# Kernel optimization log

Hardware: AMD Instinct MI355X
Metric: run time of the kernel (lower is better)

Reference implementation:

```python
import jax, jax.numpy as jnp
import numpy as np

N_NODES = 100000
N_EDGES = 3200000
N_FEAT = 128
HIDDEN = 64
N_CLASSES = 3
N_GRAPHS = 512
BN_EPS = 1e-5


def setup_inputs() -> dict:
    key = jax.random.key(0)
    ks = jax.random.split(key, 16)
    x = jax.random.normal(ks[0], (N_NODES, N_FEAT), dtype=jnp.float32)
    edge_index = jax.random.randint(ks[1], (2, N_EDGES), 0, N_NODES, dtype=jnp.int64)
    batch = jnp.sort(jax.random.randint(ks[2], (N_NODES,), 0, N_GRAPHS, dtype=jnp.int64))
    # GCNConv weights (glorot-ish scale), biases
    W1 = jax.random.normal(ks[3], (N_FEAT, HIDDEN), dtype=jnp.float32) / np.sqrt(N_FEAT)
    b1 = jnp.zeros((HIDDEN,), dtype=jnp.float32)
    W2 = jax.random.normal(ks[4], (HIDDEN, HIDDEN), dtype=jnp.float32) / np.sqrt(HIDDEN)
    b2 = jnp.zeros((HIDDEN,), dtype=jnp.float32)
    # BatchNorm params + running stats (eval mode)
    g1 = jnp.ones((HIDDEN,), dtype=jnp.float32)
    bt1 = jnp.zeros((HIDDEN,), dtype=jnp.float32)
    rm1 = jax.random.normal(ks[5], (HIDDEN,), dtype=jnp.float32) * 0.1
    rv1 = jax.random.uniform(ks[6], (HIDDEN,), dtype=jnp.float32) + 0.5
    g2 = jnp.ones((HIDDEN,), dtype=jnp.float32)
    bt2 = jnp.zeros((HIDDEN,), dtype=jnp.float32)
    rm2 = jax.random.normal(ks[7], (HIDDEN,), dtype=jnp.float32) * 0.1
    rv2 = jax.random.uniform(ks[8], (HIDDEN,), dtype=jnp.float32) + 0.5
    # classifier
    Wc = jax.random.normal(ks[9], (HIDDEN, N_CLASSES), dtype=jnp.float32) / np.sqrt(HIDDEN)
    bc = jnp.zeros((N_CLASSES,), dtype=jnp.float32)
    return dict(x=x, W1=W1, b1=b1, g1=g1, bt1=bt1, rm1=rm1, rv1=rv1,
                W2=W2, b2=b2, g2=g2, bt2=bt2, rm2=rm2, rv2=rv2,
                Wc=Wc, bc=bc, edge_index=edge_index, batch=batch)


def _gcn_conv(x, W, b, src, dst):
    # x' = D^{-1/2} (A + I) D^{-1/2} X W + b  (PyG GCNConv with self-loops)
    n = x.shape[0]
    h = x @ W  # [N, H]
    loops = jnp.arange(n, dtype=src.dtype)
    s = jnp.concatenate([src, loops])
    d = jnp.concatenate([dst, loops])
    deg = jax.ops.segment_sum(jnp.ones_like(d, dtype=h.dtype), d, num_segments=n)
    dinv = jnp.where(deg > 0, jax.lax.rsqrt(deg), 0.0)
    norm = dinv[s] * dinv[d]  # [E+N]
    msg = h[s] * norm[:, None]  # gather + scale
    out = jax.ops.segment_sum(msg, d, num_segments=n)  # scatter-add
    return out + b


def _bn_eval(x, gamma, beta, rmean, rvar):
    return (x - rmean) * jax.lax.rsqrt(rvar + BN_EPS) * gamma + beta


def reference(x, W1, b1, g1, bt1, rm1, rv1, W2, b2, g2, bt2, rm2, rv2, Wc, bc, edge_index, batch):
    src, dst = edge_index[0], edge_index[1]
    h = _gcn_conv(x, W1, b1, src, dst)
    h = jax.nn.relu(_bn_eval(h, g1, bt1, rm1, rv1))
    # dropout inactive in eval mode
    h = _gcn_conv(h, W2, b2, src, dst)
    h = jax.nn.relu(_bn_eval(h, g2, bt2, rm2, rv2))
    # global mean pool over graphs
    sums = jax.ops.segment_sum(h, batch, num_segments=N_GRAPHS)
    cnts = jax.ops.segment_sum(jnp.ones((h.shape[0],), dtype=h.dtype), batch, num_segments=N_GRAPHS)
    pooled = sums / jnp.maximum(cnts, 1.0)[:, None]  # [G, H]
    return pooled @ Wc + bc  # [G, C]
```

## Files before the change

### kernel.cpp

```cpp
#include <hip/hip_runtime.h>

#define NN 100000
#define NE 3200000
#define NG 512
#define NCB 782
#define BN_EPS 1e-5f

typedef unsigned short u16;
typedef unsigned int u32;

__device__ __forceinline__ u16 f2bf(float f) {
    u32 u = __float_as_uint(f);
    u += 0x7FFF + ((u >> 16) & 1);
    return (u16)(u >> 16);
}

__global__ __launch_bounds__(256) void k_chist(const int* __restrict__ dst, int* __restrict__ ccount) {
    __shared__ int h[NCB];
    int t = threadIdx.x;
    for (int i = t; i < NCB; i += 256) h[i] = 0;
    __syncthreads();
    int stride = gridDim.x * 256;
    for (int e = blockIdx.x * 256 + t; e < NE; e += stride)
        atomicAdd(&h[dst[e] >> 7], 1);
    __syncthreads();
    for (int i = t; i < NCB; i += 256)
        if (h[i]) atomicAdd(&ccount[i], h[i]);
}

__global__ __launch_bounds__(256) void k_cscan(const int* __restrict__ ccount, int* __restrict__ cbase,
                                               int* __restrict__ fbase, int* __restrict__ gcur) {
    __shared__ int sh[256], sh2[256];
    int t = threadIdx.x;
    int v[4], w[4];
    int s = 0, s2 = 0;
#pragma unroll
    for (int j = 0; j < 4; j++) {
        int idx = t * 4 + j;
        int c = (idx < NCB) ? ccount[idx] : 0;
        v[j] = c;
        w[j] = (idx < NCB) ? ((c + 387) & ~3) : 0;
        s += v[j]; s2 += w[j];
    }
    sh[t] = s; sh2[t] = s2;
    __syncthreads();
    for (int off = 1; off < 256; off <<= 1) {
        int x = (t >= off) ? sh[t - off] : 0;
        int x2 = (t >= off) ? sh2[t - off] : 0;
        __syncthreads();
        sh[t] += x; sh2[t] += x2;
        __syncthreads();
    }
    int run = sh[t] - s, run2 = sh2[t] - s2;
#pragma unroll
    for (int j = 0; j < 4; j++) {
        int idx = t * 4 + j;
        if (idx < NCB) { cbase[idx] = run; gcur[idx] = run; fbase[idx] = run2; }
        run += v[j]; run2 += w[j];
    }
    if (t == 255) cbase[NCB] = run;
}

#define P1_CHUNK 16384
__global__ __launch_bounds__(1024) void k_p1(const int* __restrict__ src, const int* __restrict__ dst,
                                             int* __restrict__ gcur, int* __restrict__ esc) {
    __shared__ int ccur[NCB];
    const int t = threadIdx.x;
    const int e0 = blockIdx.x * P1_CHUNK;
    for (int i = t; i < NCB; i += 1024) ccur[i] = 0;
    __syncthreads();
    int n = NE - e0; if (n > P1_CHUNK) n = P1_CHUNK;
    for (int idx = t; idx < n; idx += 1024)
        atomicAdd(&ccur[dst[e0 + idx] >> 7], 1);
    __syncthreads();
    for (int i = t; i < NCB; i += 1024) {
        int c = ccur[i];
        ccur[i] = (c > 0) ? atomicAdd(&gcur[i], c) : 0;
    }
    __syncthreads();
    for (int idx = t; idx < n; idx += 1024) {
        int dd = dst[e0 + idx];
        int s = src[e0 + idx];
        int pos = atomicAdd(&ccur[dd >> 7], 1);
        esc[pos] = s | ((dd & 127) << 17);
    }
}

__global__ __launch_bounds__(256) void k_p2(const int* __restrict__ esc, const int* __restrict__ cbase,
                                            const int* __restrict__ fbase, int* __restrict__ esf,
                                            int* __restrict__ offs, int* __restrict__ cntp,
                                            float* __restrict__ dinv) {
    __shared__ int lcnt[128], loff[128], lcur[128];
    int t = threadIdx.x, b = blockIdx.x;
    int c0 = cbase[b], c1 = cbase[b + 1];
    if (t < 128) lcnt[t] = 0;
    __syncthreads();
    for (int i = c0 + t; i < c1; i += 256) atomicAdd(&lcnt[esc[i] >> 17], 1);
    __syncthreads();
    int p = 0, cnt = 0;
    if (t < 128) { cnt = lcnt[t]; p = (cnt + 3) & ~3; loff[t] = p; }
    __syncthreads();
    for (int off = 1; off < 128; off <<= 1) {
        int x = (t >= off && t < 128) ? loff[t - off] : 0;
        __syncthreads();
        if (t < 128) loff[t] += x;
        __syncthreads();
    }
    int fb = fbase[b];
    int node = (b << 7) + t;
    if (t < 128) {
        int o = fb + loff[t] - p;
        lcur[t] = o;
        if (node < NN) {
            offs[node] = o;
            cntp[node] = p;
            dinv[node] = rsqrtf((float)(cnt + 1));
            for (int q = cnt; q < p; q++) esf[o + q] = NN;
        }
    }
    __syncthreads();
    for (int i = c0 + t; i < c1; i += 256) {
        int rec = esc[i];
        int pos = atomicAdd(&lcur[rec >> 17], 1);
        esf[pos] = rec & 0x1FFFF;
    }
}

template <int K>
__global__ __launch_bounds__(256) void k_gemm(const float* __restrict__ X,
                                              const float* __restrict__ W,
                                              const float* __restrict__ dinv,
                                              u16* __restrict__ hp, int M) {
    __shared__ float xs[128 * 68];
    __shared__ float ws[64 * 64];
    const int t = threadIdx.x;
    const int row0 = blockIdx.x * 128;
    const int rg = t >> 3;
    const int f0 = (t & 7) * 8;

    float acc[4][8];
#pragma unroll
    for (int j = 0; j < 4; j++)
#pragma unroll
        for (int c = 0; c < 8; c++) acc[j][c] = 0.0f;

    for (int kc = 0; kc < K; kc += 64) {
        __syncthreads();
        const float4* Wg = (const float4*)(W + (size_t)kc * 64);
        float4* ws4 = (float4*)ws;
#pragma unroll
        for (int i = 0; i < 4; i++) ws4[t + i * 256] = Wg[t + i * 256];
#pragma unroll
        for (int p = 0; p < 8; p++) {
            int rr = p * 16 + (t >> 4);
            int c4 = (t & 15) * 4;
            int row = row0 + rr;
            float4 v = make_float4(0.f, 0.f, 0.f, 0.f);
            if (row < M) v = *(const float4*)(X + (size_t)row * K + kc + c4);
            *(float4*)(&xs[rr * 68 + c4]) = v;
        }
        __syncthreads();

        for (int kk = 0; kk < 64; kk += 4) {
            float4 xv[4];
#pragma unroll
            for (int j = 0; j < 4; j++)
                xv[j] = *(const float4*)(&xs[(rg + 32 * j) * 68 + kk]);
#pragma unroll
            for (int kki = 0; kki < 4; kki++) {
                float4 w0 = *(const float4*)(&ws[(kk + kki) * 64 + f0]);
                float4 w1 = *(const float4*)(&ws[(kk + kki) * 64 + f0 + 4]);
#pragma unroll
                for (int j = 0; j < 4; j++) {
                    float a = (&xv[j].x)[kki];
                    acc[j][0] = fmaf(a, w0.x, acc[j][0]);
                    acc[j][1] = fmaf(a, w0.y, acc[j][1]);
                    acc[j][2] = fmaf(a, w0.z, acc[j][2]);
                    acc[j][3] = fmaf(a, w0.w, acc[j][3]);
                    acc[j][4] = fmaf(a, w1.x, acc[j][4]);
                    acc[j][5] = fmaf(a, w1.y, acc[j][5]);
                    acc[j][6] = fmaf(a, w1.z, acc[j][6]);
                    acc[j][7] = fmaf(a, w1.w, acc[j][7]);
                }
            }
        }
    }

#pragma unroll
    for (int j = 0; j < 4; j++) {
        int row = row0 + rg + 32 * j;
        if (row < M) {
            float di = dinv[row];
            uint4 pk;
            pk.x = (u32)f2bf(acc[j][0] * di) | ((u32)f2bf(acc[j][1] * di) << 16);
            pk.y = (u32)f2bf(acc[j][2] * di) | ((u32)f2bf(acc[j][3] * di) << 16);
            pk.z = (u32)f2bf(acc[j][4] * di) | ((u32)f2bf(acc[j][5] * di) << 16);
            pk.w = (u32)f2bf(acc[j][6] * di) | ((u32)f2bf(acc[j][7] * di) << 16);
            *(uint4*)(hp + (size_t)row * 64 + f0) = pk;
        }
    }
}

__global__ __launch_bounds__(256) void k_agg(const u32* __restrict__ hp2,
                                             const int* __restrict__ esf,
                                             const int* __restrict__ offs,
                                             const int* __restrict__ cntp,
                                             const float* __restrict__ dinv,
                                             const float* __restrict__ bias,
                                             const float* __restrict__ gam,
                                             const float* __restrict__ bet,
                                             const float* __restrict__ rm,
                                             const float* __restrict__ rv,
                                             float* __restrict__ out) {
    const int lane = threadIdx.x & 63;
    const int half = lane >> 5;
    const int fp = lane & 31;
    const int node = (blockIdx.x * 256 + threadIdx.x) >> 6;
    if (node >= NN) return;
    const int beg = offs[node];
    const int mp = cntp[node];
    float ax = 0.0f, ay = 0.0f;
    for (int c = 0; c < mp; c += 64) {
        int m = mp - c;
        if (m > 64) m = 64;
        int rec = (lane < m) ? esf[beg + c + lane] : NN;
        int j = 0;
        for (; j + 16 <= m; j += 16) {
            u32 v[8];
#pragma unroll
            for (int u = 0; u < 8; u++) {
                int s = __shfl(rec, j + 2 * u + half);
                v[u] = hp2[(size_t)s * 32 + fp];
            }
#pragma unroll
            for (int u = 0; u < 8; u++) {
                ax += __uint_as_float(v[u] << 16);
                ay += __uint_as_float(v[u] & 0xFFFF0000u);
            }
        }
        for (; j < m; j += 4) {
            int s0 = __shfl(rec, j + half);
            int s1 = __shfl(rec, j + 2 + half);
            u32 v0 = hp2[(size_t)s0 * 32 + fp];
            u32 v1 = hp2[(size_t)s1 * 32 + fp];
            ax += __uint_as_float(v0 << 16);
            ay += __uint_as_float(v0 & 0xFFFF0000u);
            ax += __uint_as_float(v1 << 16);
            ay += __uint_as_float(v1 & 0xFFFF0000u);
        }
    }
    ax += __shfl_xor(ax, 32);
    ay += __shfl_xor(ay, 32);
    u32 sv = hp2[(size_t)node * 32 + fp];
    ax += __uint_as_float(sv << 16);
    ay += __uint_as_float(sv & 0xFFFF0000u);

    const float di = dinv[node];
    const int f0 = fp * 2;
    float2 bia = *(const float2*)(bias + f0);
    float2 ga  = *(const float2*)(gam + f0);
    float2 be  = *(const float2*)(bet + f0);
    float2 rme = *(const float2*)(rm + f0);
    float2 rva = *(const float2*)(rv + f0);
    float vx = ax * di + bia.x;
    float vy = ay * di + bia.y;
    float yx = (vx - rme.x) * (ga.x * rsqrtf(rva.x + BN_EPS)) + be.x;
    float yy = (vy - rme.y) * (ga.y * rsqrtf(rva.y + BN_EPS)) + be.y;
    if (half == 0)
        *(float2*)(out + (size_t)node * 64 + f0) = make_float2(fmaxf(yx, 0.0f), fmaxf(yy, 0.0f));
}

__global__ __launch_bounds__(256) void k_poolcls(const float* __restrict__ h,
                                                 const int* __restrict__ batch,
                                                 const float* __restrict__ Wc,
                                                 const float* __restrict__ bc,
                                                 float* __restrict__ out) {
    __shared__ float sh[256];
    const int g = blockIdx.x;
    const int t = threadIdx.x;
    const int lane = t & 63;
    const int wv = t >> 6;
    int lo = 0, hi = NN;
    while (lo < hi) { int mid = (lo + hi) >> 1; if (batch[mid] < g) lo = mid + 1; else hi = mid; }
    const int r0 = lo;
    hi = NN;
    while (lo < hi) { int mid = (lo + hi) >> 1; if (batch[mid] < g + 1) lo = mid + 1; else hi = mid; }
    const int r1 = lo;
    float acc = 0.0f;
    for (int r = r0 + wv; r < r1; r += 4)
        acc += h[(size_t)r * 64 + lane];
    sh[t] = acc;
    __syncthreads();
    if (wv == 0) {
        float p = sh[lane] + sh[64 + lane] + sh[128 + lane] + sh[192 + lane];
        p *= 1.0f / fmaxf((float)(r1 - r0), 1.0f);
        float c0 = p * Wc[lane * 3 + 0];
        float c1 = p * Wc[lane * 3 + 1];
        float c2 = p * Wc[lane * 3 + 2];
        for (int o = 32; o > 0; o >>= 1) {
            c0 += __shfl_xor(c0, o);
            c1 += __shfl_xor(c1, o);
            c2 += __shfl_xor(c2, o);
        }
        if (lane == 0) {
            out[g * 3 + 0] = c0 + bc[0];
            out[g * 3 + 1] = c1 + bc[1];
            out[g * 3 + 2] = c2 + bc[2];
        }
    }
}

extern "C" void kernel_launch(void* const* d_in, const int* in_sizes, int n_in,
                              void* d_out, int out_size, void* d_ws, size_t ws_size,
                              hipStream_t stream) {
    const float* x   = (const float*)d_in[0];
    const float* W1  = (const float*)d_in[1];
    const float* b1  = (const float*)d_in[2];
    const float* g1  = (const float*)d_in[3];
    const float* bt1 = (const float*)d_in[4];
    const float* rm1 = (const float*)d_in[5];
    const float* rv1 = (const float*)d_in[6];
    const float* W2  = (const float*)d_in[7];
    const float* b2  = (const float*)d_in[8];
    const float* g2  = (const float*)d_in[9];
    const float* bt2 = (const float*)d_in[10];
    const float* rm2 = (const float*)d_in[11];
    const float* rv2 = (const float*)d_in[12];
    const float* Wc  = (const float*)d_in[13];
    const float* bc  = (const float*)d_in[14];
    const int* ei    = (const int*)d_in[15];
    const int* batch = (const int*)d_in[16];
    const int* srcp = ei;
    const int* dstp = ei + NE;

    char* ws = (char*)d_ws;
    u16*   hpb    = (u16*)(ws);
    int*   ccount = (int*)(ws + 12800128);
    int*   cbase  = (int*)(ws + 12803264);
    int*   fbase  = (int*)(ws + 12806400);
    int*   gcur   = (int*)(ws + 12809536);
    int*   offs   = (int*)(ws + 12812672);
    int*   cntp   = (int*)(ws + 13212672);
    float* dinv   = (float*)(ws + 13612672);
    int*   esf    = (int*)(ws + 14012672);
    float* bufB   = (float*)(ws + 28052672);
    int*   esc    = (int*)(ws + 28052672);

    hipMemsetAsync(hpb + (size_t)NN * 64, 0, 128 + NCB * 4, stream);

    k_chist<<<512, 256, 0, stream>>>(dstp, ccount);
    k_cscan<<<1, 256, 0, stream>>>(ccount, cbase, fbase, gcur);
    k_p1<<<(NE + P1_CHUNK - 1) / P1_CHUNK, 1024, 0, stream>>>(srcp, dstp, gcur, esc);
    k_p2<<<NCB, 256, 0, stream>>>(esc, cbase, fbase, esf, offs, cntp, dinv);

    k_gemm<128><<<(NN + 127) / 128, 256, 0, stream>>>(x, W1, dinv, hpb, NN);
    k_agg<<<(NN * 64 + 255) / 256, 256, 0, stream>>>((const u32*)hpb, esf, offs, cntp, dinv, b1, g1, bt1, rm1, rv1, bufB);

    k_gemm<64><<<(NN + 127) / 128, 256, 0, stream>>>(bufB, W2, dinv, hpb, NN);
    k_agg<<<(NN * 64 + 255) / 256, 256, 0, stream>>>((const u32*)hpb, esf, offs, cntp, dinv, b2, g2, bt2, rm2, rv2, bufB);

    k_poolcls<<<NG, 256, 0, stream>>>(bufB, batch, Wc, bc, (float*)d_out);
}
```

Baseline: 394.4 us.

## Fuse CSR build kernels into one cooperative kernel with grid syncs

Replaces the four graph-build kernels (coarse histogram, scan, coarse scatter, fine bucket sort) with a single cooperative kernel of 196 blocks of 1024 threads. Grid-wide barriers separate the phases. The per-block histogram is kept in shared memory and reused for the scatter pass, so dst is read once fewer. In the fine phase each block handles four coarse buckets with 256-thread subgroups. The aim is to remove launch gaps and a redundant pass. The cost is grid.sync overhead, lower parallelism in phase 2 (196 blocks instead of 782), and a single-block scan.

Measured after the change: 488.9 us. 24.0% more time.

```diff
diff --git a/kernel.cpp b/kernel.cpp
--- a/kernel.cpp
+++ b/kernel.cpp
@@ -1,4 +1,7 @@
 #include <hip/hip_runtime.h>
+#include <hip/hip_cooperative_groups.h>
+
+namespace cg = cooperative_groups;
 
 #define NN 100000
 #define NE 3200000
@@ -6,6 +9,9 @@
 #define NCB 782
 #define BN_EPS 1e-5f
 
+#define BCHUNK 16384
+#define NBLK 196
+
 typedef unsigned short u16;
 typedef unsigned int u32;
 
@@ -15,114 +21,106 @@
     return (u16)(u >> 16);
 }
 
-__global__ __launch_bounds__(256) void k_chist(const int* __restrict__ dst, int* __restrict__ ccount) {
-    __shared__ int h[NCB];
-    int t = threadIdx.x;
-    for (int i = t; i < NCB; i += 256) h[i] = 0;
+__global__ __launch_bounds__(1024) void k_build(const int* __restrict__ src, const int* __restrict__ dst,
+                                                int* __restrict__ ccount, int* __restrict__ cbase,
+                                                int* __restrict__ fbase, int* __restrict__ gcur,
+                                                int* __restrict__ esc, int* __restrict__ esf,
+                                                int* __restrict__ offs, int* __restrict__ cntp,
+                                                float* __restrict__ dinv) {
+    __shared__ int lhist[NCB];
+    __shared__ int buf[2048];
+    cg::grid_group grid = cg::this_grid();
+    const int t = threadIdx.x;
+    const int b = blockIdx.x;
+    const int e0 = b * BCHUNK;
+    int n = NE - e0; if (n > BCHUNK) n = BCHUNK; if (n < 0) n = 0;
+
+    for (int i = t; i < NCB; i += 1024) lhist[i] = 0;
     __syncthreads();
-    int stride = gridDim.x * 256;
-    for (int e = blockIdx.x * 256 + t; e < NE; e += stride)
-        atomicAdd(&h[dst[e] >> 7], 1);
+    for (int idx = t; idx < n; idx += 1024)
+        atomicAdd(&lhist[dst[e0 + idx] >> 7], 1);
     __syncthreads();
-    for (int i = t; i < NCB; i += 256)
-        if (h[i]) atomicAdd(&ccount[i], h[i]);
-}
-
-__global__ __launch_bounds__(256) void k_cscan(const int* __restrict__ ccount, int* __restrict__ cbase,
-                                               int* __restrict__ fbase, int* __restrict__ gcur) {
-    __shared__ int sh[256], sh2[256];
-    int t = threadIdx.x;
-    int v[4], w[4];
-    int s = 0, s2 = 0;
-#pragma unroll
-    for (int j = 0; j < 4; j++) {
-        int idx = t * 4 + j;
-        int c = (idx < NCB) ? ccount[idx] : 0;
-        v[j] = c;
-        w[j] = (idx < NCB) ? ((c + 387) & ~3) : 0;
-        s += v[j]; s2 += w[j];
-    }
-    sh[t] = s; sh2[t] = s2;
-    __syncthreads();
-    for (int off = 1; off < 256; off <<= 1) {
-        int x = (t >= off) ? sh[t - off] : 0;
-        int x2 = (t >= off) ? sh2[t - off] : 0;
-        __syncthreads();
-        sh[t] += x; sh2[t] += x2;
-        __syncthreads();
-    }
-    int run = sh[t] - s, run2 = sh2[t] - s2;
-#pragma unroll
-    for (int j = 0; j < 4; j++) {
-        int idx = t * 4 + j;
-        if (idx < NCB) { cbase[idx] = run; gcur[idx] = run; fbase[idx] = run2; }
-        run += v[j]; run2 += w[j];
-    }
-    if (t == 255) cbase[NCB] = run;
-}
-
-#define P1_CHUNK 16384
-__global__ __launch_bounds__(1024) void k_p1(const int* __restrict__ src, const int* __restrict__ dst,
-                                             int* __restrict__ gcur, int* __restrict__ esc) {
-    __shared__ int ccur[NCB];
-    const int t = threadIdx.x;
-    const int e0 = blockIdx.x * P1_CHUNK;
-    for (int i = t; i < NCB; i += 1024) ccur[i] = 0;
-    __syncthreads();
-    int n = NE - e0; if (n > P1_CHUNK) n = P1_CHUNK;
-    for (int idx = t; idx < n; idx += 1024)
-        atomicAdd(&ccur[dst[e0 + idx] >> 7], 1);
-    __syncthreads();
+    for (int i = t; i < NCB; i += 1024)
+        if (lhist[i]) atomicAdd(&ccount[i], lhist[i]);
+
+    grid.sync();
+
+    if (b == 0) {
+        int v = 0, w = 0;
+        if (t < NCB) { v = ccount[t]; w = (v + 387) & ~3; }
+        buf[t] = v; buf[1024 + t] = w;
+        __syncthreads();
+        for (int off = 1; off < 1024; off <<= 1) {
+            int x = (t >= off) ? buf[t - off] : 0;
+            int x2 = (t >= off) ? buf[1024 + t - off] : 0;
+            __syncthreads();
+            buf[t] += x; buf[1024 + t] += x2;
+            __syncthreads();
+        }
+        if (t < NCB) {
+            cbase[t] = buf[t] - v;
+            gcur[t]  = buf[t] - v;
+            fbase[t] = buf[1024 + t] - w;
+        }
+        if (t == 0) cbase[NCB] = NE;
+    }
+
+    grid.sync();
+
     for (int i = t; i < NCB; i += 1024) {
-        int c = ccur[i];
-        ccur[i] = (c > 0) ? atomicAdd(&gcur[i], c) : 0;
+        int c = lhist[i];
+        lhist[i] = (c > 0) ? atomicAdd(&gcur[i], c) : 0;
     }
     __syncthreads();
     for (int idx = t; idx < n; idx += 1024) {
         int dd = dst[e0 + idx];
         int s = src[e0 + idx];
-        int pos = atomicAdd(&ccur[dd >> 7], 1);
+        int pos = atomicAdd(&lhist[dd >> 7], 1);
         esc[pos] = s | ((dd & 127) << 17);
     }
-}
-
-__global__ __launch_bounds__(256) void k_p2(const int* __restrict__ esc, const int* __restrict__ cbase,
-                                            const int* __restrict__ fbase, int* __restrict__ esf,
-                                            int* __restrict__ offs, int* __restrict__ cntp,
-                                            float* __restrict__ dinv) {
-    __shared__ int lcnt[128], loff[128], lcur[128];
-    int t = threadIdx.x, b = blockIdx.x;
-    int c0 = cbase[b], c1 = cbase[b + 1];
-    if (t < 128) lcnt[t] = 0;
-    __syncthreads();
-    for (int i = c0 + t; i < c1; i += 256) atomicAdd(&lcnt[esc[i] >> 17], 1);
-    __syncthreads();
-    int p = 0, cnt = 0;
-    if (t < 128) { cnt = lcnt[t]; p = (cnt + 3) & ~3; loff[t] = p; }
-    __syncthreads();
-    for (int off = 1; off < 128; off <<= 1) {
-        int x = (t >= off && t < 128) ? loff[t - off] : 0;
-        __syncthreads();
-        if (t < 128) loff[t] += x;
-        __syncthreads();
-    }
-    int fb = fbase[b];
-    int node = (b << 7) + t;
-    if (t < 128) {
-        int o = fb + loff[t] - p;
-        lcur[t] = o;
-        if (node < NN) {
-            offs[node] = o;
-            cntp[node] = p;
-            dinv[node] = rsqrtf((float)(cnt + 1));
-            for (int q = cnt; q < p; q++) esf[o + q] = NN;
-        }
-    }
-    __syncthreads();
-    for (int i = c0 + t; i < c1; i += 256) {
-        int rec = esc[i];
-        int pos = atomicAdd(&lcur[rec >> 17], 1);
-        esf[pos] = rec & 0x1FFFF;
+
+    grid.sync();
+
+    {
+        const int g = t >> 8;
+        const int tl = t & 255;
+        const int bk = b * 4 + g;
+        int* lcnt = buf + g * 512;
+        int* loff = lcnt + 128;
+        int* lcur = loff + 128;
+        const bool act = bk < NCB;
+        int c0 = 0, c1 = 0, fb = 0;
+        if (act) { c0 = cbase[bk]; c1 = cbase[bk + 1]; fb = fbase[bk]; }
+        if (tl < 128) lcnt[tl] = 0;
+        __syncthreads();
+        if (act) for (int i = c0 + tl; i < c1; i += 256) atomicAdd(&lcnt[esc[i] >> 17], 1);
+        __syncthreads();
+        int p = 0, cnt = 0;
+        if (tl < 128) { cnt = lcnt[tl]; p = (cnt + 3) & ~3; loff[tl] = p; }
+        __syncthreads();
+        for (int off = 1; off < 128; off <<= 1) {
+            int x = (tl >= off && tl < 128) ? loff[tl - off] : 0;
+            __syncthreads();
+            if (tl < 128) loff[tl] += x;
+            __syncthreads();
+        }
+        const int node = (bk << 7) + tl;
+        if (act && tl < 128) {
+            int o = fb + loff[tl] - p;
+            lcur[tl] = o;
+            if (node < NN) {
+                offs[node] = o;
+                cntp[node] = p;
+                dinv[node] = rsqrtf((float)(cnt + 1));
+                for (int q = cnt; q < p; q++) esf[o + q] = NN;
+            }
+        }
+        __syncthreads();
+        if (act) for (int i = c0 + tl; i < c1; i += 256) {
+            int rec = esc[i];
+            int pos = atomicAdd(&lcur[rec >> 17], 1);
+            esf[pos] = rec & 0x1FFFF;
+        }
     }
 }
 
@@ -348,10 +346,11 @@
 
     hipMemsetAsync(hpb + (size_t)NN * 64, 0, 128 + NCB * 4, stream);
 
-    k_chist<<<512, 256, 0, stream>>>(dstp, ccount);
-    k_cscan<<<1, 256, 0, stream>>>(ccount, cbase, fbase, gcur);
-    k_p1<<<(NE + P1_CHUNK - 1) / P1_CHUNK, 1024, 0, stream>>>(srcp, dstp, gcur, esc);
-    k_p2<<<NCB, 256, 0, stream>>>(esc, cbase, fbase, esf, offs, cntp, dinv);
+    {
+        void* args[] = {(void*)&srcp, (void*)&dstp, (void*)&ccount, (void*)&cbase, (void*)&fbase,
+                        (void*)&gcur, (void*)&esc, (void*)&esf, (void*)&offs, (void*)&cntp, (void*)&dinv};
+        hipLaunchCooperativeKernel((void*)k_build, dim3(NBLK), dim3(1024), args, 0, stream);
+    }
 
     k_gemm<128><<<(NN + 127) / 128, 256, 0, stream>>>(x, W1, dinv, hpb, NN);
     k_agg<<<(NN * 64 + 255) / 256, 256, 0, stream>>>((const u32*)hpb, esf, offs, cntp, dinv, b1, g1, bt1, rm1, rv1, bufB);
```
